# Kernel tuning notes

Measured on AMD Instinct MI355X. Metric: run time of the kernel, lower is better.

The kernel has to match this reference:

```python
import jax, jax.numpy as jnp
import numpy as np

DENSE_W = 0.7  # unused in learned fusion path but kept for parity
SPARSE_W = 0.3

def _l2norm(x):
    return x / jnp.linalg.norm(x, axis=-1, keepdims=True)

def setup_inputs() -> dict:
    key = jax.random.key(0)
    ks = jax.random.split(key, 8)
    Q, D, dim = 32, 4096, 384
    feat = 2 * dim + 2  # 770
    query_dense = _l2norm(jax.random.normal(ks[0], (Q, dim), jnp.float32))
    doc_dense = _l2norm(jax.random.normal(ks[1], (D, dim), jnp.float32))
    sparse_scores = jax.random.uniform(ks[2], (Q, D), jnp.float32)
    W1 = jax.random.normal(ks[3], (feat, 384), jnp.float32) * (1.0 / np.sqrt(feat))
    b1 = jnp.zeros((384,), jnp.float32)
    W2 = jax.random.normal(ks[4], (384, 192), jnp.float32) * (1.0 / np.sqrt(384))
    b2 = jnp.zeros((192,), jnp.float32)
    W3 = jax.random.normal(ks[5], (192, 1), jnp.float32) * (1.0 / np.sqrt(192))
    b3 = jnp.zeros((1,), jnp.float32)
    return {"query_dense": query_dense, "doc_dense": doc_dense,
            "sparse_scores": sparse_scores,
            "W1": W1, "b1": b1, "W2": W2, "b2": b2, "W3": W3, "b3": b3}

def reference(query_dense, doc_dense, sparse_scores, W1, b1, W2, b2, W3, b3):
    # dense cosine similarity (inputs are L2-normalized): [Q, D]
    dense_scores = query_dense @ doc_dense.T
    Q, D = dense_scores.shape
    dim = query_dense.shape[1]
    # Vectorized equivalent of the per-pair gather+concat double loop:
    # feature[q, d] = [query_dense[q], doc_dense[d], dense[q,d], sparse[q,d]]
    qf = jnp.broadcast_to(query_dense[:, None, :], (Q, D, dim))
    df = jnp.broadcast_to(doc_dense[None, :, :], (Q, D, dim))
    features = jnp.concatenate(
        [qf, df, dense_scores[..., None], sparse_scores[..., None]], axis=-1)  # [Q, D, 2*dim+2]
    # 4-layer fusion MLP (Dropout is identity at inference)
    h = jax.nn.relu(features @ W1 + b1)
    h = jax.nn.relu(h @ W2 + b2)
    fusion_weights = jax.nn.sigmoid((h @ W3 + b3)[..., 0])  # [Q, D]
    final_scores = fusion_weights * dense_scores + (1.0 - fusion_weights) * sparse_scores
    return final_scores, dense_scores, sparse_scores
```

## Files before the change

### kernel.cpp

```cpp
#include <hip/hip_runtime.h>
#include <hip/hip_bf16.h>

typedef __attribute__((ext_vector_type(4)))  float f32x4;
typedef __attribute__((ext_vector_type(16))) float f32x16;
typedef __attribute__((ext_vector_type(8)))  short bf16x8;

__device__ __forceinline__ short f2bf(float x){
    __hip_bfloat16 h = __float2bfloat16(x);
    return __builtin_bit_cast(short, h);
}
__device__ __forceinline__ float bf2f(short x){
    unsigned int u = ((unsigned int)(unsigned short)x) << 16;
    return __builtin_bit_cast(float, u);
}

__global__ __launch_bounds__(256)
void pre_kernel(const float* __restrict__ query, const float* __restrict__ doc,
                const float* __restrict__ sparse, const float* __restrict__ W1,
                const float* __restrict__ b1,
                float* __restrict__ out_dense, float* __restrict__ out_sparse,
                short* __restrict__ Bws, float* __restrict__ Aq, short* __restrict__ W1cd){
    __shared__ float ldsq[32*388];
    __shared__ float ldsd[16*388];
    const int b = blockIdx.x, tid = threadIdx.x;

    if (b < 256){
        const int d0 = b*16;
        #pragma unroll
        for (int i=0;i<12;i++){ int idx = tid + i*256; int row = idx/96, c4 = idx%96;
            *(f32x4*)(ldsq + row*388 + c4*4) = *(const f32x4*)(query + row*384 + c4*4); }
        #pragma unroll
        for (int i=0;i<6;i++){ int idx = tid + i*256; int row = idx/96, c4 = idx%96;
            *(f32x4*)(ldsd + row*388 + c4*4) = *(const f32x4*)(doc + (d0+row)*384 + c4*4); }
        __syncthreads();
        const int q = tid>>3, dg = tid&7;
        float acc0 = 0.0f, acc1 = 0.0f;
        #pragma unroll 4
        for (int k=0;k<384;k++){
            float qv = ldsq[q*388 + k];
            acc0 += qv*ldsd[dg*388 + k];
            acc1 += qv*ldsd[(dg+8)*388 + k];
        }
        out_dense[q*4096 + d0 + dg]     = acc0;
        out_dense[q*4096 + d0 + dg + 8] = acc1;
        if (tid < 128){
            int qq = tid>>2, c4 = tid&3;
            *(f32x4*)(out_sparse + qq*4096 + d0 + c4*4) = *(const f32x4*)(sparse + qq*4096 + d0 + c4*4);
        }
    } else if (b < 514){
        const int bb = b - 256;
        const int w = tid >> 6, lane = tid & 63;
        const int cl = lane & 15, quad = lane >> 4;
        const float* src; const float* wrow; int r0; bool isA;
        if (bb < 256){ r0 = bb*16;       src = doc;   wrow = W1 + 384*384; isA = false; }
        else         { r0 = (bb-256)*16; src = query; wrow = W1;           isA = true;  }

        f32x4 acc[6];
        #pragma unroll
        for (int t=0;t<6;t++) acc[t] = (f32x4){0.f,0.f,0.f,0.f};

        #pragma unroll 1
        for (int s=0;s<12;s++){
            const float* ap = src + (r0+cl)*384 + s*32 + quad*8;
            const f32x4 a0 = *(const f32x4*)ap;
            const f32x4 a1 = *(const f32x4*)(ap+4);
            bf16x8 af;
            #pragma unroll
            for (int j=0;j<4;j++){ af[j] = f2bf(a0[j]); af[4+j] = f2bf(a1[j]); }
            const float* wk = wrow + (s*32 + quad*8)*384;
            #pragma unroll
            for (int tt=0;tt<6;tt++){
                const int col = (w*6+tt)*16 + cl;
                bf16x8 bf_;
                #pragma unroll
                for (int j=0;j<8;j++) bf_[j] = f2bf(wk[j*384 + col]);
                acc[tt] = __builtin_amdgcn_mfma_f32_16x16x32_bf16(af, bf_, acc[tt], 0, 0, 0);
            }
        }
        #pragma unroll
        for (int tt=0;tt<6;tt++){
            const int col = (w*6+tt)*16 + cl;
            if (isA){
                const float b1v = b1[col];
                #pragma unroll
                for (int r=0;r<4;r++)
                    Aq[(r0 + quad*4 + r)*384 + col] = acc[tt][r] + b1v;
            } else {
                #pragma unroll
                for (int r=0;r<4;r++)
                    Bws[(r0 + quad*4 + r)*384 + col] = f2bf(acc[tt][r]);
            }
        }
    } else {
        #pragma unroll
        for (int i=0;i<3;i++){
            int o3 = tid + i*256;
            int k = (o3>>4)*8 + (o3&7);
            int which = (o3>>3)&1;
            W1cd[o3] = f2bf(W1[(768+which)*384 + k]);
        }
    }
}

__global__ __launch_bounds__(512, 2)
void main_kernel(const float* __restrict__ Aq, const short* __restrict__ Bws,
                 const short* __restrict__ W1cd,
                 const float* __restrict__ b2, const float* __restrict__ W3,
                 const float* __restrict__ b3, const float* __restrict__ sparse,
                 const float* __restrict__ W2, const float* __restrict__ dense_in,
                 float* __restrict__ out_final){
    __shared__ short lw[73728];
    const int tid = threadIdx.x;
    #pragma unroll
    for (int i=0;i<18;i++){
        int c = tid + i*512;
        int lane_c = c & 63, st = c >> 6;
        int s = st/6, t2 = st%6;
        int n = t2*32 + (lane_c&31), kb = s*16 + ((lane_c>>5)&1)*8;
        bf16x8 v;
        #pragma unroll
        for (int j=0;j<8;j++) v[j] = f2bf(W2[(kb+j)*192 + n]);
        *(bf16x8*)(lw + c*8) = v;
    }
    __syncthreads();

    const int lane = tid & 63, w = tid >> 6;
    const int m = lane & 31, q2 = lane >> 5;
    const int kbase = q2*8;
    const float b3v = b3[0];

    #pragma unroll 1
    for (int t4=0; t4<2; t4++){
        const int dcol = blockIdx.x*16 + t4*8 + w;
        const float dsv = dense_in[m*4096 + dcol];
        const float ssv = sparse[m*4096 + dcol];

        f32x16 acc[6];
        #pragma unroll
        for (int t=0;t<6;t++)
            #pragma unroll
            for (int r=0;r<16;r++) acc[t][r] = 0.0f;

        bf16x8 bw_c = *(const bf16x8*)(Bws + dcol*384 + kbase);
        f32x4  a0_c = *(const f32x4*)(Aq + m*384 + kbase);
        f32x4  a1_c = *(const f32x4*)(Aq + m*384 + kbase + 4);

        #pragma unroll 1
        for (int s=0;s<24;s++){
            const int k0 = s*16 + kbase;
            const int kn = (s < 23) ? (k0 + 16) : kbase;
            const bf16x8 bw_n = *(const bf16x8*)(Bws + dcol*384 + kn);
            const f32x4  a0_n = *(const f32x4*)(Aq + m*384 + kn);
            const f32x4  a1_n = *(const f32x4*)(Aq + m*384 + kn + 4);
            const bf16x8 wcv = *(const bf16x8*)(W1cd + (s*2 + q2)*16);
            const bf16x8 wdv = *(const bf16x8*)(W1cd + (s*2 + q2)*16 + 8);
            bf16x8 fr;
            #pragma unroll
            for (int j=0;j<4;j++){
                float h0 = a0_c[j] + bf2f(bw_c[j])   + dsv*bf2f(wcv[j])   + ssv*bf2f(wdv[j]);
                float h1 = a1_c[j] + bf2f(bw_c[4+j]) + dsv*bf2f(wcv[4+j]) + ssv*bf2f(wdv[4+j]);
                fr[j]   = f2bf(fmaxf(h0, 0.0f));
                fr[4+j] = f2bf(fmaxf(h1, 0.0f));
            }
            #pragma unroll
            for (int t=0;t<6;t++){
                const bf16x8 bfr = *(const bf16x8*)(lw + ((s*6 + t)*64 + lane)*8);
                acc[t] = __builtin_amdgcn_mfma_f32_32x32x16_bf16(fr, bfr, acc[t], 0, 0, 0);
            }
            bw_c = bw_n; a0_c = a0_n; a1_c = a1_n;
        }

        float p[16];
        #pragma unroll
        for (int r=0;r<16;r++) p[r] = 0.0f;
        #pragma unroll
        for (int t=0;t<6;t++){
            const int n = t*32 + m;
            const float b2v = b2[n];
            const float w3v = W3[n];
            #pragma unroll
            for (int r=0;r<16;r++)
                p[r] += fmaxf(acc[t][r] + b2v, 0.0f) * w3v;
        }
        #pragma unroll
        for (int mask=1; mask<32; mask<<=1){
            #pragma unroll
            for (int r=0;r<16;r++) p[r] += __shfl_xor(p[r], mask);
        }
        float myp = p[0];
        #pragma unroll
        for (int r=1;r<16;r++) myp = (m==r) ? p[r] : myp;
        if (m < 16){
            const int row = (m&3) + 8*(m>>2) + 4*q2;
            float logit = myp + b3v;
            float wgt = 1.0f/(1.0f + __expf(-logit));
            float dd = dense_in[row*4096 + dcol];
            float ss = sparse[row*4096 + dcol];
            out_final[row*4096 + dcol] = wgt*dd + (1.0f - wgt)*ss;
        }
    }
}

extern "C" void kernel_launch(void* const* d_in, const int* in_sizes, int n_in,
                              void* d_out, int out_size, void* d_ws, size_t ws_size,
                              hipStream_t stream){
    const float* query  = (const float*)d_in[0];
    const float* doc    = (const float*)d_in[1];
    const float* sparse = (const float*)d_in[2];
    const float* W1     = (const float*)d_in[3];
    const float* b1     = (const float*)d_in[4];
    const float* W2     = (const float*)d_in[5];
    const float* b2     = (const float*)d_in[6];
    const float* W3     = (const float*)d_in[7];
    const float* b3     = (const float*)d_in[8];

    float* out_final  = (float*)d_out;
    float* out_dense  = (float*)d_out + 131072;
    float* out_sparse = (float*)d_out + 262144;

    short* Bws  = (short*)d_ws;
    float* Aq   = (float*)((char*)d_ws + 3145728);
    short* W1cd = (short*)((char*)d_ws + 3194880);

    hipLaunchKernelGGL(pre_kernel,  dim3(515), dim3(256), 0, stream,
                       query, doc, sparse, W1, b1, out_dense, out_sparse, Bws, Aq, W1cd);
    hipLaunchKernelGGL(main_kernel, dim3(256), dim3(512), 0, stream,
                       Aq, Bws, W1cd, b2, W3, b3, sparse, W2, out_dense, out_final);
}
```

Measured before the change: 134.8 us.

## Split layer-2 N across two wave groups and pre-pack W2 once in pre_kernel

The main kernel now runs 1024 threads per block, and each pair of waves splits the 192 layer-2 output columns in half. Their partial logits are reduced through shared memory before the sigmoid blend. The bf16 swizzle of W2 moves into extra pre_kernel blocks, so every main block copies a ready packed buffer instead of converting W2 per block. The W1 dense/sparse weight rows are now kept in fp32 in LDS, and the dense dot product is vectorised to float4. The aim is more waves to hide latency and less redundant per-block prep, at the cost of two extra block barriers per iteration and duplicated layer-1 feature computation across the two wave groups.

```diff
diff --git a/kernel.cpp b/kernel.cpp
--- a/kernel.cpp
+++ b/kernel.cpp
@@ -17,9 +17,10 @@
 __global__ __launch_bounds__(256)
 void pre_kernel(const float* __restrict__ query, const float* __restrict__ doc,
                 const float* __restrict__ sparse, const float* __restrict__ W1,
-                const float* __restrict__ b1,
+                const float* __restrict__ b1, const float* __restrict__ W2,
                 float* __restrict__ out_dense, float* __restrict__ out_sparse,
-                short* __restrict__ Bws, float* __restrict__ Aq, short* __restrict__ W1cd){
+                short* __restrict__ Bws, float* __restrict__ Aq,
+                float* __restrict__ W1cdf, short* __restrict__ W2t){
     __shared__ float ldsq[32*388];
     __shared__ float ldsd[16*388];
     const int b = blockIdx.x, tid = threadIdx.x;
@@ -34,15 +35,18 @@
             *(f32x4*)(ldsd + row*388 + c4*4) = *(const f32x4*)(doc + (d0+row)*384 + c4*4); }
         __syncthreads();
         const int q = tid>>3, dg = tid&7;
-        float acc0 = 0.0f, acc1 = 0.0f;
+        const f32x4* q4  = (const f32x4*)(ldsq + q*388);
+        const f32x4* d4a = (const f32x4*)(ldsd + dg*388);
+        const f32x4* d4b = (const f32x4*)(ldsd + (dg+8)*388);
+        f32x4 s0 = {0.f,0.f,0.f,0.f}, s1 = {0.f,0.f,0.f,0.f};
         #pragma unroll 4
-        for (int k=0;k<384;k++){
-            float qv = ldsq[q*388 + k];
-            acc0 += qv*ldsd[dg*388 + k];
-            acc1 += qv*ldsd[(dg+8)*388 + k];
-        }
-        out_dense[q*4096 + d0 + dg]     = acc0;
-        out_dense[q*4096 + d0 + dg + 8] = acc1;
+        for (int k=0;k<96;k++){
+            const f32x4 qv = q4[k];
+            s0 += qv*d4a[k];
+            s1 += qv*d4b[k];
+        }
+        out_dense[q*4096 + d0 + dg]     = s0[0]+s0[1]+s0[2]+s0[3];
+        out_dense[q*4096 + d0 + dg + 8] = s1[0]+s1[1]+s1[2]+s1[3];
         if (tid < 128){
             int qq = tid>>2, c4 = tid&3;
             *(f32x4*)(out_sparse + qq*4096 + d0 + c4*4) = *(const f32x4*)(sparse + qq*4096 + d0 + c4*4);
@@ -91,53 +95,63 @@
                     Bws[(r0 + quad*4 + r)*384 + col] = f2bf(acc[tt][r]);
             }
         }
+    } else if (b == 514){
+        #pragma unroll
+        for (int i=0;i<3;i++){
+            int o = tid + i*256;
+            W1cdf[o] = (o < 384) ? W1[768*384 + o] : W1[769*384 + (o - 384)];
+        }
     } else {
-        #pragma unroll
-        for (int i=0;i<3;i++){
-            int o3 = tid + i*256;
-            int k = (o3>>4)*8 + (o3&7);
-            int which = (o3>>3)&1;
-            W1cd[o3] = f2bf(W1[(768+which)*384 + k]);
+        const int t0 = (b - 515)*256 + tid;
+        #pragma unroll
+        for (int i=0;i<9;i++){
+            int c = t0 + i*1024;
+            int lane_c = c & 63, st = c >> 6;
+            int s = st/6, t2 = st%6;
+            int n = t2*32 + (lane_c&31), kb = s*16 + ((lane_c>>5)&1)*8;
+            bf16x8 v;
+            #pragma unroll
+            for (int j=0;j<8;j++) v[j] = f2bf(W2[(kb+j)*192 + n]);
+            *(bf16x8*)(W2t + c*8) = v;
         }
     }
 }
 
-__global__ __launch_bounds__(512, 2)
+__global__ __launch_bounds__(1024, 4)
 void main_kernel(const float* __restrict__ Aq, const short* __restrict__ Bws,
-                 const short* __restrict__ W1cd,
+                 const float* __restrict__ W1cdf, const short* __restrict__ W2t,
                  const float* __restrict__ b2, const float* __restrict__ W3,
                  const float* __restrict__ b3, const float* __restrict__ sparse,
-                 const float* __restrict__ W2, const float* __restrict__ dense_in,
-                 float* __restrict__ out_final){
-    __shared__ short lw[73728];
+                 const float* __restrict__ dense_in, float* __restrict__ out_final){
+    __shared__ __align__(16) short lw[73728];
+    __shared__ __align__(16) float lcd[768];
+    __shared__ float lred[512];
     const int tid = threadIdx.x;
+
     #pragma unroll
-    for (int i=0;i<18;i++){
-        int c = tid + i*512;
-        int lane_c = c & 63, st = c >> 6;
-        int s = st/6, t2 = st%6;
-        int n = t2*32 + (lane_c&31), kb = s*16 + ((lane_c>>5)&1)*8;
-        bf16x8 v;
-        #pragma unroll
-        for (int j=0;j<8;j++) v[j] = f2bf(W2[(kb+j)*192 + n]);
-        *(bf16x8*)(lw + c*8) = v;
+    for (int i=0;i<9;i++){
+        int c = tid + i*1024;
+        *(f32x4*)(lw + c*8) = *(const f32x4*)(W2t + c*8);
     }
+    if (tid < 192)
+        *(f32x4*)(lcd + tid*4) = *(const f32x4*)(W1cdf + tid*4);
     __syncthreads();
 
     const int lane = tid & 63, w = tid >> 6;
+    const int wc = w & 7, ngrp = w >> 3;
     const int m = lane & 31, q2 = lane >> 5;
     const int kbase = q2*8;
     const float b3v = b3[0];
 
     #pragma unroll 1
     for (int t4=0; t4<2; t4++){
-        const int dcol = blockIdx.x*16 + t4*8 + w;
+        const int dcol = blockIdx.x*16 + t4*8 + wc;
         const float dsv = dense_in[m*4096 + dcol];
         const float ssv = sparse[m*4096 + dcol];
 
-        f32x16 acc[6];
-        #pragma unroll
-        for (int t=0;t<6;t++)
+        f32x16 acc[3];
+        #pragma unroll
+        for (int t=0;t<3;t++)
             #pragma unroll
             for (int r=0;r<16;r++) acc[t][r] = 0.0f;
 
@@ -152,20 +166,23 @@
             const bf16x8 bw_n = *(const bf16x8*)(Bws + dcol*384 + kn);
             const f32x4  a0_n = *(const f32x4*)(Aq + m*384 + kn);
             const f32x4  a1_n = *(const f32x4*)(Aq + m*384 + kn + 4);
-            const bf16x8 wcv = *(const bf16x8*)(W1cd + (s*2 + q2)*16);
-            const bf16x8 wdv = *(const bf16x8*)(W1cd + (s*2 + q2)*16 + 8);
+            const f32x4 wc0 = *(const f32x4*)(lcd + k0);
+            const f32x4 wc1 = *(const f32x4*)(lcd + k0 + 4);
+            const f32x4 wd0 = *(const f32x4*)(lcd + 384 + k0);
+            const f32x4 wd1 = *(const f32x4*)(lcd + 384 + k0 + 4);
             bf16x8 fr;
             #pragma unroll
             for (int j=0;j<4;j++){
-                float h0 = a0_c[j] + bf2f(bw_c[j])   + dsv*bf2f(wcv[j])   + ssv*bf2f(wdv[j]);
-                float h1 = a1_c[j] + bf2f(bw_c[4+j]) + dsv*bf2f(wcv[4+j]) + ssv*bf2f(wdv[4+j]);
+                float h0 = a0_c[j] + bf2f(bw_c[j])   + dsv*wc0[j] + ssv*wd0[j];
+                float h1 = a1_c[j] + bf2f(bw_c[4+j]) + dsv*wc1[j] + ssv*wd1[j];
                 fr[j]   = f2bf(fmaxf(h0, 0.0f));
                 fr[4+j] = f2bf(fmaxf(h1, 0.0f));
             }
             #pragma unroll
-            for (int t=0;t<6;t++){
+            for (int tt=0;tt<3;tt++){
+                const int t = ngrp*3 + tt;
                 const bf16x8 bfr = *(const bf16x8*)(lw + ((s*6 + t)*64 + lane)*8);
-                acc[t] = __builtin_amdgcn_mfma_f32_32x32x16_bf16(fr, bfr, acc[t], 0, 0, 0);
+                acc[tt] = __builtin_amdgcn_mfma_f32_32x32x16_bf16(fr, bfr, acc[tt], 0, 0, 0);
             }
             bw_c = bw_n; a0_c = a0_n; a1_c = a1_n;
         }
@@ -174,13 +191,13 @@
         #pragma unroll
         for (int r=0;r<16;r++) p[r] = 0.0f;
         #pragma unroll
-        for (int t=0;t<6;t++){
-            const int n = t*32 + m;
+        for (int tt=0;tt<3;tt++){
+            const int n = (ngrp*3 + tt)*32 + m;
             const float b2v = b2[n];
             const float w3v = W3[n];
             #pragma unroll
             for (int r=0;r<16;r++)
-                p[r] += fmaxf(acc[t][r] + b2v, 0.0f) * w3v;
+                p[r] += fmaxf(acc[tt][r] + b2v, 0.0f) * w3v;
         }
         #pragma unroll
         for (int mask=1; mask<32; mask<<=1){
@@ -192,12 +209,19 @@
         for (int r=1;r<16;r++) myp = (m==r) ? p[r] : myp;
         if (m < 16){
             const int row = (m&3) + 8*(m>>2) + 4*q2;
-            float logit = myp + b3v;
-            float wgt = 1.0f/(1.0f + __expf(-logit));
-            float dd = dense_in[row*4096 + dcol];
-            float ss = sparse[row*4096 + dcol];
-            out_final[row*4096 + dcol] = wgt*dd + (1.0f - wgt)*ss;
-        }
+            lred[wc*64 + row*2 + ngrp] = myp;
+        }
+        __syncthreads();
+        if (tid < 256){
+            const int cl = tid >> 5, row = tid & 31;
+            const float logit = lred[cl*64 + row*2] + lred[cl*64 + row*2 + 1] + b3v;
+            const float wgt = 1.0f/(1.0f + __expf(-logit));
+            const int dc = blockIdx.x*16 + t4*8 + cl;
+            const float dd = dense_in[row*4096 + dc];
+            const float ss = sparse[row*4096 + dc];
+            out_final[row*4096 + dc] = wgt*dd + (1.0f - wgt)*ss;
+        }
+        __syncthreads();
     }
 }
 
@@ -218,12 +242,13 @@
     float* out_dense  = (float*)d_out + 131072;
     float* out_sparse = (float*)d_out + 262144;
 
-    short* Bws  = (short*)d_ws;
-    float* Aq   = (float*)((char*)d_ws + 3145728);
-    short* W1cd = (short*)((char*)d_ws + 3194880);
-
-    hipLaunchKernelGGL(pre_kernel,  dim3(515), dim3(256), 0, stream,
-                       query, doc, sparse, W1, b1, out_dense, out_sparse, Bws, Aq, W1cd);
-    hipLaunchKernelGGL(main_kernel, dim3(256), dim3(512), 0, stream,
-                       Aq, Bws, W1cd, b2, W3, b3, sparse, W2, out_dense, out_final);
-}
+    short* Bws   = (short*)d_ws;
+    float* Aq    = (float*)((char*)d_ws + 3145728);
+    float* W1cdf = (float*)((char*)d_ws + 3194880);
+    short* W2t   = (short*)((char*)d_ws + 3197952);
+
+    hipLaunchKernelGGL(pre_kernel,  dim3(519), dim3(256), 0, stream,
+                       query, doc, sparse, W1, b1, W2, out_dense, out_sparse, Bws, Aq, W1cdf, W2t);
+    hipLaunchKernelGGL(main_kernel, dim3(256), dim3(1024), 0, stream,
+                       Aq, Bws, W1cdf, W2t, b2, W3, b3, sparse, out_dense, out_final);
+}
```

After: 154.8 us. 14.9% more time.
